# Kernel optimization log

Measured on AMD Instinct MI355X. Metric: run time of the kernel, lower is better.

## Reference

```python
import jax, jax.numpy as jnp
import numpy as np

N = 100_000      # nodes
E = 1_600_000    # edges (avg degree 16)
D = 64           # input_dim == hidden_dim
C = 10           # output classes
G = 512          # graphs in batch
L = 5            # num_layers (L-1 = 4 GINConv layers)
BN_EPS = 1e-5


def setup_inputs() -> dict:
    key = jax.random.key(0)
    ks = jax.random.split(key, 16)
    x = jax.random.normal(ks[0], (N, D), dtype=jnp.float32)
    edge_index = jax.random.randint(ks[1], (2, E), 0, N, dtype=jnp.int32)
    batch = jnp.sort(jax.random.randint(ks[2], (N,), 0, G, dtype=jnp.int32))
    s = 1.0 / np.sqrt(D)
    Lc = L - 1
    return {
        "x": x,
        "edge_index": edge_index,
        "batch": batch,
        "eps": jnp.zeros((Lc,), jnp.float32),                                   # GINConv eps (train_eps, init 0)
        "W1": jax.random.uniform(ks[3], (Lc, D, D), jnp.float32, -s, s),        # MLP linear 1
        "b1": jax.random.uniform(ks[4], (Lc, D), jnp.float32, -s, s),
        "g1": jnp.ones((Lc, D), jnp.float32),                                   # MLP BatchNorm
        "be1": jnp.zeros((Lc, D), jnp.float32),
        "W2": jax.random.uniform(ks[5], (Lc, D, D), jnp.float32, -s, s),        # MLP linear 2
        "b2": jax.random.uniform(ks[6], (Lc, D), jnp.float32, -s, s),
        "gout": jnp.ones((Lc, D), jnp.float32),                                 # outer BatchNorm
        "beout": jnp.zeros((Lc, D), jnp.float32),
        "Wp": jax.random.uniform(ks[7], (L, D, C), jnp.float32, -s, s),         # prediction linears
        "bp": jax.random.uniform(ks[8], (L, C), jnp.float32, -s, s),
    }


def _batchnorm(h, gamma, beta):
    # training-mode BN over node dim, biased variance (torch semantics)
    m = jnp.mean(h, axis=0)
    v = jnp.mean(jnp.square(h - m), axis=0)
    return gamma * (h - m) * jax.lax.rsqrt(v + BN_EPS) + beta


def reference(x, edge_index, batch, eps, W1, b1, g1, be1, W2, b2, gout, beout, Wp, bp):
    src, dst = edge_index[0], edge_index[1]
    hidden_rep = [x]
    h = x
    for l in range(L - 1):
        # GINConv: (1 + eps) * x + scatter-add of neighbor features
        agg = jax.ops.segment_sum(h[src], dst, num_segments=N)
        z = (1.0 + eps[l]) * h + agg
        # 2-layer MLP with internal BN+ReLU
        z = z @ W1[l] + b1[l]
        z = jax.nn.relu(_batchnorm(z, g1[l], be1[l]))
        z = z @ W2[l] + b2[l]
        # outer BN + ReLU
        h = jax.nn.relu(_batchnorm(z, gout[l], beout[l]))
        hidden_rep.append(h)
    # jumping-knowledge readout: per-layer global_add_pool + linear (dropout off / eval)
    score = jnp.zeros((G, C), jnp.float32)
    for l, hl in enumerate(hidden_rep):
        pooled = jax.ops.segment_sum(hl, batch, num_segments=G)
        score = score + pooled @ Wp[l] + bp[l]
    return score
```

## Files before the change

### kernel.cpp

```cpp
#include <hip/hip_runtime.h>

#define NN 100000
#define EE 1600000
#define DD 64
#define CC 10
#define GG 512
#define LL 5
#define NPAD 100352
#define N64 (NN * DD)
#define NB 392
#define PCH 4096
#define BCAP 6144
#define SC 8

typedef short bf16x8 __attribute__((ext_vector_type(8)));
typedef float f32x4  __attribute__((ext_vector_type(4)));
union U16 { uint4 u; bf16x8 h; };

__device__ __forceinline__ float bits2f(unsigned int b) { return __uint_as_float(b); }
__device__ __forceinline__ float bf2f(unsigned short s) { return __uint_as_float((unsigned int)s << 16); }
__device__ __forceinline__ unsigned short f2bf_rne(float v) {
    unsigned int b = __float_as_uint(v);
    return (unsigned short)((b + 0x7fffu + ((b >> 16) & 1u)) >> 16);
}
__device__ __forceinline__ void unpack8(uint4 u, float* f) {
    f[0] = bits2f(u.x << 16); f[1] = bits2f(u.x & 0xffff0000u);
    f[2] = bits2f(u.y << 16); f[3] = bits2f(u.y & 0xffff0000u);
    f[4] = bits2f(u.z << 16); f[5] = bits2f(u.z & 0xffff0000u);
    f[6] = bits2f(u.w << 16); f[7] = bits2f(u.w & 0xffff0000u);
}
__device__ __forceinline__ uint4 pack8(const float* f) {
    uint4 u;
    u.x = (unsigned int)f2bf_rne(f[0]) | ((unsigned int)f2bf_rne(f[1]) << 16);
    u.y = (unsigned int)f2bf_rne(f[2]) | ((unsigned int)f2bf_rne(f[3]) << 16);
    u.z = (unsigned int)f2bf_rne(f[4]) | ((unsigned int)f2bf_rne(f[5]) << 16);
    u.w = (unsigned int)f2bf_rne(f[6]) | ((unsigned int)f2bf_rne(f[7]) << 16);
    return u;
}
__device__ __forceinline__ void acc8(uint4 u, float* a) {
    float t[8];
    unpack8(u, t);
    #pragma unroll
    for (int k = 0; k < 8; ++k) a[k] += t[k];
}

__global__ __launch_bounds__(256) void prep_x_pool_k(
    const float* __restrict__ x, const int* __restrict__ batch,
    unsigned short* __restrict__ hb, float* __restrict__ pooled)
{
    int t = threadIdx.x;
    int f = t & 63;
    int q = t >> 6;
    int n0 = blockIdx.x * 64 + q * 16;
    int nmax = NN - n0; if (nmax > 16) nmax = 16;
    float acc = 0.f;
    int curg = -1;
    #pragma unroll 4
    for (int i = 0; i < nmax; ++i) {
        int n = n0 + i;
        int g = batch[n];
        if (g != curg) {
            if (curg >= 0) atomicAdd(&pooled[(size_t)curg * DD + f], acc);
            acc = 0.f; curg = g;
        }
        float v = x[(size_t)n * DD + f];
        hb[(size_t)n * DD + f] = f2bf_rne(v);
        acc += v;
    }
    if (curg >= 0) atomicAdd(&pooled[(size_t)curg * DD + f], acc);
}

__global__ __launch_bounds__(256) void prep_w_k(const float* __restrict__ W1,
                                                const float* __restrict__ W2,
                                                unsigned short* __restrict__ wt) {
    int mat = blockIdx.x;
    const float* src = (mat < 4) ? (W1 + (size_t)mat * 4096)
                                 : (W2 + (size_t)(mat - 4) * 4096);
    for (int idx = threadIdx.x; idx < 4096; idx += 256) {
        int c = idx >> 6, k = idx & 63;
        wt[(size_t)mat * 4096 + c * 64 + k] = f2bf_rne(src[k * 64 + c]);
    }
}

__global__ __launch_bounds__(256) void bhist_k(const int* __restrict__ ei,
                                               int* __restrict__ bh) {
    __shared__ int cnt[NB];
    for (int i = threadIdx.x; i < NB; i += 256) cnt[i] = 0;
    __syncthreads();
    int stride = gridDim.x * 256;
    for (int e = blockIdx.x * 256 + threadIdx.x; e < EE; e += stride)
        atomicAdd(&cnt[ei[EE + e] >> 8], 1);
    __syncthreads();
    for (int i = threadIdx.x; i < NB; i += 256)
        if (cnt[i]) atomicAdd(&bh[i], cnt[i]);
}

__global__ __launch_bounds__(512) void bscan_k(const int* __restrict__ bh,
                                               int* __restrict__ bo,
                                               int* __restrict__ bcur) {
    __shared__ int s[512];
    int t = threadIdx.x;
    int v = (t < NB) ? bh[t] : 0;
    s[t] = v;
    __syncthreads();
    for (int d = 1; d < 512; d <<= 1) {
        int a = (t >= d) ? s[t - d] : 0;
        __syncthreads();
        s[t] += a;
        __syncthreads();
    }
    int excl = s[t] - v;
    if (t < NB) { bo[t] = excl; bcur[t] = excl; }
    if (t == NB - 1) bo[NB] = excl + v;
}

__global__ __launch_bounds__(256) void partition_k(const int* __restrict__ ei,
                                                   int* __restrict__ bcur,
                                                   unsigned int* __restrict__ stage) {
    __shared__ int hist[NB];
    __shared__ int base[NB];
    __shared__ int gbase[NB];
    __shared__ int cnt2[NB];
    __shared__ int scanbuf[512];
    __shared__ unsigned int pairs[PCH];
    __shared__ unsigned short pbkt[PCH];
    int t = threadIdx.x;
    int e0 = blockIdx.x * PCH;
    int nE = EE - e0; if (nE > PCH) nE = PCH;

    for (int i = t; i < NB; i += 256) { hist[i] = 0; cnt2[i] = 0; }
    __syncthreads();

    int mys[16], myd[16];
    #pragma unroll
    for (int i = 0; i < 16; ++i) {
        int idx = i * 256 + t;
        if (idx < nE) {
            mys[i] = ei[e0 + idx];
            myd[i] = ei[EE + e0 + idx];
            atomicAdd(&hist[myd[i] >> 8], 1);
        } else myd[i] = -1;
    }
    __syncthreads();

    scanbuf[t]       = (t < NB) ? hist[t] : 0;
    scanbuf[t + 256] = (t + 256 < NB) ? hist[t + 256] : 0;
    __syncthreads();
    for (int d = 1; d < 512; d <<= 1) {
        int a0 = (t >= d) ? scanbuf[t - d] : 0;
        int a1 = ((t + 256) >= d) ? scanbuf[t + 256 - d] : 0;
        __syncthreads();
        scanbuf[t] += a0;
        scanbuf[t + 256] += a1;
        __syncthreads();
    }
    if (t < NB)       base[t]       = scanbuf[t] - hist[t];
    if (t + 256 < NB) base[t + 256] = scanbuf[t + 256] - hist[t + 256];
    __syncthreads();

    #pragma unroll
    for (int i = 0; i < 16; ++i) {
        if (myd[i] >= 0) {
            int b = myd[i] >> 8;
            int p = base[b] + atomicAdd(&cnt2[b], 1);
            pairs[p] = (unsigned)mys[i] | ((unsigned)(myd[i] & 255) << 17);
            pbkt[p] = (unsigned short)b;
        }
    }
    __syncthreads();
    for (int i = t; i < NB; i += 256)
        if (hist[i]) gbase[i] = atomicAdd(&bcur[i], hist[i]);
    __syncthreads();
    for (int p = t; p < nE; p += 256) {
        int b = pbkt[p];
        stage[gbase[b] + (p - base[b])] = pairs[p];
    }
}

__global__ __launch_bounds__(256) void bucket_csr_k(const unsigned int* __restrict__ stage,
                                                    const int* __restrict__ bo,
                                                    int* __restrict__ adj,
                                                    int* __restrict__ offs) {
    __shared__ int deg[256];
    __shared__ int sb[256];
    __shared__ int nb_[256];
    __shared__ int c2[256];
    __shared__ int loc[BCAP];
    int b = blockIdx.x;
    int s0 = bo[b], s1 = bo[b + 1];
    int cnt = s1 - s0;
    int t = threadIdx.x;

    deg[t] = 0;
    __syncthreads();
    for (int i = t; i < cnt; i += 256) atomicAdd(&deg[(stage[s0 + i] >> 17) & 255], 1);
    __syncthreads();
    sb[t] = deg[t];
    __syncthreads();
    for (int d = 1; d < 256; d <<= 1) {
        int a = (t >= d) ? sb[t - d] : 0;
        __syncthreads();
        sb[t] += a;
        __syncthreads();
    }
    int nbase = sb[t] - deg[t];
    nb_[t] = nbase;
    c2[t] = 0;
    offs[b * 256 + t] = s0 + nbase;
    __syncthreads();

    if (cnt <= BCAP) {
        for (int i = t; i < cnt; i += 256) {
            unsigned int pr = stage[s0 + i];
            int ln = (pr >> 17) & 255;
            int p = nb_[ln] + atomicAdd(&c2[ln], 1);
            loc[p] = (int)(pr & 0x1FFFF);
        }
        __syncthreads();
        for (int i = t; i < cnt; i += 256) adj[s0 + i] = loc[i];
    } else {
        for (int i = t; i < cnt; i += 256) {
            unsigned int pr = stage[s0 + i];
            int ln = (pr >> 17) & 255;
            int p = nb_[ln] + atomicAdd(&c2[ln], 1);
            adj[s0 + p] = (int)(pr & 0x1FFFF);
        }
    }
}

__global__ __launch_bounds__(512, 6) void layer1_k(
    const unsigned short* __restrict__ hb, const int* __restrict__ adj,
    const int* __restrict__ offs, const float* __restrict__ epsArr, int l,
    const unsigned short* __restrict__ wtm, const float* __restrict__ bias,
    unsigned short* __restrict__ z1, float* __restrict__ stats1,
    float* __restrict__ stats2z)
{
    __shared__ unsigned short aLDS[64 * 64];
    const int t = threadIdx.x;
    const int lane = t & 63;
    const int w = t >> 6;
    const int n15 = lane & 15;
    const int quad = lane >> 4;

    if (blockIdx.x < SC && t < 128) stats2z[blockIdx.x * 128 + t] = 0.f;

    const float epsv = 1.0f + epsArr[l];
    const int c8 = lane & 7;
    {
        int lr = w * 8 + (lane >> 3);
        int n = blockIdx.x * 64 + lr;
        float acc[8] = {0.f,0.f,0.f,0.f,0.f,0.f,0.f,0.f};
        if (n < NN) {
            uint4 a = *(const uint4*)(hb + (size_t)n * DD + c8 * 8);
            unpack8(a, acc);
            #pragma unroll
            for (int j2 = 0; j2 < 8; ++j2) acc[j2] *= epsv;
            int j = offs[n], end = offs[n + 1];
            #pragma unroll 1
            for (; j + 3 < end; j += 4) {
                int s0 = adj[j], s1 = adj[j + 1], s2 = adj[j + 2], s3 = adj[j + 3];
                uint4 v0 = *(const uint4*)(hb + (size_t)s0 * DD + c8 * 8);
                uint4 v1 = *(const uint4*)(hb + (size_t)s1 * DD + c8 * 8);
                uint4 v2 = *(const uint4*)(hb + (size_t)s2 * DD + c8 * 8);
                uint4 v3 = *(const uint4*)(hb + (size_t)s3 * DD + c8 * 8);
                acc8(v0, acc); acc8(v1, acc); acc8(v2, acc); acc8(v3, acc);
            }
            #pragma unroll 1
            for (; j < end; ++j) {
                uint4 v0 = *(const uint4*)(hb + (size_t)adj[j] * DD + c8 * 8);
                acc8(v0, acc);
            }
        }
        int pu = c8 ^ (lr & 7);
        *(uint4*)(aLDS + lr * 64 + pu * 8) = pack8(acc);
    }

    const int rt = w & 3;
    const int cb = (w >> 2) * 2;
    U16 bfr[2][2];
    #pragma unroll
    for (int ci = 0; ci < 2; ++ci)
        #pragma unroll
        for (int ks = 0; ks < 2; ++ks)
            bfr[ci][ks].u = *(const uint4*)(wtm + (size_t)((cb + ci) * 16 + n15) * 64 + ks * 32 + quad * 8);

    __syncthreads();

    U16 afr[2];
    int lr2 = rt * 16 + n15;
    #pragma unroll
    for (int ks = 0; ks < 2; ++ks) {
        int pu = (ks * 4 + quad) ^ (lr2 & 7);
        afr[ks].u = *(const uint4*)(aLDS + lr2 * 64 + pu * 8);
    }

    const int rowg0 = blockIdx.x * 64 + rt * 16;
    const int copy = blockIdx.x & (SC - 1);
    #pragma unroll
    for (int ci = 0; ci < 2; ++ci) {
        int ct = cb + ci;
        f32x4 acc = {0.f, 0.f, 0.f, 0.f};
        acc = __builtin_amdgcn_mfma_f32_16x16x32_bf16(afr[0].h, bfr[ci][0].h, acc, 0, 0, 0);
        acc = __builtin_amdgcn_mfma_f32_16x16x32_bf16(afr[1].h, bfr[ci][1].h, acc, 0, 0, 0);
        int col = ct * 16 + n15;
        float bcol = bias[col];
        float s = 0.f, ss = 0.f;
        #pragma unroll
        for (int r = 0; r < 4; ++r) {
            int rg = rowg0 + quad * 4 + r;
            float v = acc[r] + bcol;
            if (rg < NN) {
                z1[(size_t)rg * DD + col] = f2bf_rne(v);
                s += v;
                ss = fmaf(v, v, ss);
            }
        }
        s  += __shfl_xor(s, 16, 64);  s  += __shfl_xor(s, 32, 64);
        ss += __shfl_xor(ss, 16, 64); ss += __shfl_xor(ss, 32, 64);
        if (lane < 16) {
            atomicAdd(&stats1[copy * 128 + ct * 16 + lane], s);
            atomicAdd(&stats1[copy * 128 + 64 + ct * 16 + lane], ss);
        }
    }
}

__global__ __launch_bounds__(256) void layer2_k(
    const unsigned short* __restrict__ z1, const float* __restrict__ stats1,
    const float* __restrict__ gamma, const float* __restrict__ beta, int off,
    const unsigned short* __restrict__ wtm, const float* __restrict__ bias,
    unsigned short* __restrict__ z2, float* __restrict__ stats2)
{
    __shared__ float ssS[128];
    const int t = threadIdx.x;
    const int lane = t & 63;
    const int w = t >> 6;
    const int n15 = lane & 15;
    const int quad = lane >> 4;
    const int rowg0 = blockIdx.x * 64 + w * 16;

    U16 bfr[4][2];
    #pragma unroll
    for (int ct = 0; ct < 4; ++ct)
        #pragma unroll
        for (int ks = 0; ks < 2; ++ks)
            bfr[ct][ks].u = *(const uint4*)(wtm + (size_t)(ct * 16 + n15) * 64 + ks * 32 + quad * 8);

    int arow = rowg0 + n15;
    int arowc = (arow < NN) ? arow : (NN - 1);
    uint4 raw[2];
    #pragma unroll
    for (int ks = 0; ks < 2; ++ks)
        raw[ks] = *(const uint4*)(z1 + (size_t)arowc * DD + ks * 32 + quad * 8);

    if (t < 64) {
        float S = 0.f, SS = 0.f;
        #pragma unroll
        for (int c = 0; c < SC; ++c) { S += stats1[c * 128 + t]; SS += stats1[c * 128 + 64 + t]; }
        float inv_n = 1.0f / (float)NN;
        float mean = S * inv_n;
        float var  = SS * inv_n - mean * mean;
        float sc = gamma[off + t] * rsqrtf(var + 1e-5f);
        ssS[t] = sc;
        ssS[64 + t] = beta[off + t] - sc * mean;
    }
    __syncthreads();

    U16 afr[2];
    #pragma unroll
    for (int ks = 0; ks < 2; ++ks) {
        float f[8];
        unpack8(raw[ks], f);
        int k0 = ks * 32 + quad * 8;
        #pragma unroll
        for (int j = 0; j < 8; ++j)
            f[j] = fmaxf(fmaf(ssS[k0 + j], f[j], ssS[64 + k0 + j]), 0.f);
        afr[ks].u = pack8(f);
    }

    const int copy = blockIdx.x & (SC - 1);
    #pragma unroll
    for (int ct = 0; ct < 4; ++ct) {
        f32x4 acc = {0.f, 0.f, 0.f, 0.f};
        acc = __builtin_amdgcn_mfma_f32_16x16x32_bf16(afr[0].h, bfr[ct][0].h, acc, 0, 0, 0);
        acc = __builtin_amdgcn_mfma_f32_16x16x32_bf16(afr[1].h, bfr[ct][1].h, acc, 0, 0, 0);
        int col = ct * 16 + n15;
        float bcol = bias[col];
        float s = 0.f, ss = 0.f;
        #pragma unroll
        for (int r = 0; r < 4; ++r) {
            int rg = rowg0 + quad * 4 + r;
            float v = acc[r] + bcol;
            if (rg < NN) {
                z2[(size_t)rg * DD + col] = f2bf_rne(v);
                s += v;
                ss = fmaf(v, v, ss);
            }
        }
        s  += __shfl_xor(s, 16, 64);  s  += __shfl_xor(s, 32, 64);
        ss += __shfl_xor(ss, 16, 64); ss += __shfl_xor(ss, 32, 64);
        if (lane < 16) {
            atomicAdd(&stats2[copy * 128 + ct * 16 + lane], s);
            atomicAdd(&stats2[copy * 128 + 64 + ct * 16 + lane], ss);
        }
    }
}

__global__ __launch_bounds__(256) void layer3_k(
    const unsigned short* __restrict__ z2, const float* __restrict__ stats2,
    const float* __restrict__ gamma, const float* __restrict__ beta, int off,
    const int* __restrict__ batch, unsigned short* __restrict__ hout,
    float* __restrict__ pooled, float* __restrict__ stats1z)
{
    __shared__ float ssS[128];
    int t = threadIdx.x;
    if (blockIdx.x < SC && t < 128) stats1z[blockIdx.x * 128 + t] = 0.f;
    if (t < 64) {
        float S = 0.f, SS = 0.f;
        #pragma unroll
        for (int c = 0; c < SC; ++c) { S += stats2[c * 128 + t]; SS += stats2[c * 128 + 64 + t]; }
        float inv_n = 1.0f / (float)NN;
        float mean = S * inv_n;
        float var  = SS * inv_n - mean * mean;
        float sc = gamma[off + t] * rsqrtf(var + 1e-5f);
        ssS[t] = sc;
        ssS[64 + t] = beta[off + t] - sc * mean;
    }
    __syncthreads();

    int f = t & 63;
    int q = t >> 6;
    int n0 = blockIdx.x * 64 + q * 16;
    int nmax = NN - n0; if (nmax > 16) nmax = 16;
    float sc = ssS[f], sh = ssS[64 + f];
    float acc = 0.f;
    int curg = -1;
    #pragma unroll 4
    for (int i = 0; i < nmax; ++i) {
        int n = n0 + i;
        int g = batch[n];
        if (g != curg) {
            if (curg >= 0) atomicAdd(&pooled[(size_t)curg * DD + f], acc);
            acc = 0.f; curg = g;
        }
        float v = bf2f(z2[(size_t)n * DD + f]);
        v = fmaxf(fmaf(sc, v, sh), 0.f);
        hout[(size_t)n * DD + f] = f2bf_rne(v);
        acc += v;
    }
    if (curg >= 0) atomicAdd(&pooled[(size_t)curg * DD + f], acc);
}

__global__ void readout_k(const float* __restrict__ pooled,
                          const float* __restrict__ Wp, const float* __restrict__ bp,
                          float* __restrict__ out)
{
    int gc = blockIdx.x * blockDim.x + threadIdx.x;
    if (gc >= GG * CC) return;
    int g = gc / CC, c = gc - g * CC;
    float acc = 0.f;
    for (int l = 0; l < LL; ++l) {
        acc += bp[l * CC + c];
        const float* p  = pooled + ((size_t)l * GG + g) * DD;
        const float* wv = Wp + (size_t)l * DD * CC + c;
        #pragma unroll 8
        for (int f = 0; f < DD; ++f) acc = fmaf(p[f], wv[f * CC], acc);
    }
    out[gc] = acc;
}

extern "C" void kernel_launch(void* const* d_in, const int* in_sizes, int n_in,
                              void* d_out, int out_size, void* d_ws, size_t ws_size,
                              hipStream_t stream) {
    const float* x     = (const float*)d_in[0];
    const int*   ei    = (const int*)d_in[1];
    const int*   batch = (const int*)d_in[2];
    const float* eps   = (const float*)d_in[3];
    const float* W1    = (const float*)d_in[4];
    const float* b1    = (const float*)d_in[5];
    const float* g1    = (const float*)d_in[6];
    const float* be1   = (const float*)d_in[7];
    const float* W2    = (const float*)d_in[8];
    const float* b2    = (const float*)d_in[9];
    const float* gout  = (const float*)d_in[10];
    const float* beout = (const float*)d_in[11];
    const float* Wp    = (const float*)d_in[12];
    const float* bp    = (const float*)d_in[13];
    float* out = (float*)d_out;

    unsigned int* stage = (unsigned int*)d_ws;
    int* adj   = (int*)(stage + EE);
    int* offs  = adj + EE;
    int* bh    = offs + NPAD + 256;
    int* bo    = bh + 400;
    int* bcur  = bo + 400;
    float* pooled = (float*)(bcur + 400);
    float* stats1 = pooled + (size_t)LL * GG * DD;
    float* stats2 = stats1 + SC * 128;
    unsigned short* hb  = (unsigned short*)(stats2 + SC * 128);
    unsigned short* z1b = hb + N64;
    unsigned short* z2b = z1b + N64;
    unsigned short* wt  = z2b + N64;

    hipMemsetAsync(pooled, 0, ((size_t)LL * GG * DD + 2 * SC * 128) * sizeof(float), stream);
    prep_x_pool_k<<<(NN + 63) / 64, 256, 0, stream>>>(x, batch, hb, pooled);
    prep_w_k<<<8, 256, 0, stream>>>(W1, W2, wt);

    hipMemsetAsync(bh, 0, NB * sizeof(int), stream);
    bhist_k<<<512, 256, 0, stream>>>(ei, bh);
    bscan_k<<<1, 512, 0, stream>>>(bh, bo, bcur);
    partition_k<<<(EE + PCH - 1) / PCH, 256, 0, stream>>>(ei, bcur, stage);
    bucket_csr_k<<<NB, 256, 0, stream>>>(stage, bo, adj, offs);

    const int gemm_grid = (NN + 63) / 64;
    const int node_grid = (NN + 63) / 64;
    for (int l = 0; l < LL - 1; ++l) {
        layer1_k<<<gemm_grid, 512, 0, stream>>>(
            hb, adj, offs, eps, l, wt + (size_t)l * 4096, b1 + l * DD, z1b, stats1, stats2);
        layer2_k<<<gemm_grid, 256, 0, stream>>>(
            z1b, stats1, g1, be1, l * DD, wt + (size_t)(4 + l) * 4096, b2 + l * DD, z2b, stats2);
        layer3_k<<<node_grid, 256, 0, stream>>>(
            z2b, stats2, gout, beout, l * DD, batch, hb,
            pooled + (size_t)(l + 1) * GG * DD, stats1);
    }
    readout_k<<<(GG * CC + 255) / 256, 256, 0, stream>>>(pooled, Wp, bp, out);
}
```

Before: 615.7 us.

## Process nodes in degree-sorted order in aggregation kernel to balance wavefront work

Builds a degree histogram during CSR construction, scans it, and scatters node ids into a permutation sorted by descending degree. The fused aggregation+GEMM kernel then processes nodes in this permuted order and writes z1 rows back to their original positions. The goal is to reduce load imbalance between lanes and waves that gather differing neighbor counts. The cost is two extra small kernels, a perm lookup, and scattered rather than contiguous row stores and self-feature reads.

```diff
diff --git a/kernel.cpp b/kernel.cpp
--- a/kernel.cpp
+++ b/kernel.cpp
@@ -180,7 +180,8 @@
 __global__ __launch_bounds__(256) void bucket_csr_k(const unsigned int* __restrict__ stage,
                                                     const int* __restrict__ bo,
                                                     int* __restrict__ adj,
-                                                    int* __restrict__ offs) {
+                                                    int* __restrict__ offs,
+                                                    int* __restrict__ dh) {
     __shared__ int deg[256];
     __shared__ int sb[256];
     __shared__ int nb_[256];
@@ -207,6 +208,10 @@
     nb_[t] = nbase;
     c2[t] = 0;
     offs[b * 256 + t] = s0 + nbase;
+    if (b * 256 + t < NN) {
+        int dgc = deg[t]; if (dgc > 127) dgc = 127;
+        atomicAdd(&dh[dgc], 1);
+    }
     __syncthreads();
 
     if (cnt <= BCAP) {
@@ -228,14 +233,38 @@
     }
 }
 
+__global__ void dscan_k(const int* __restrict__ dh, int* __restrict__ dbase) {
+    __shared__ int s[128];
+    int t = threadIdx.x;
+    s[t] = dh[t];
+    __syncthreads();
+    int sum = 0;
+    for (int d = t + 1; d < 128; ++d) sum += s[d];
+    dbase[t] = sum;
+}
+
+__global__ __launch_bounds__(256) void dscatter_k(const int* __restrict__ offs,
+                                                  int* __restrict__ dcnt,
+                                                  const int* __restrict__ dbase,
+                                                  int* __restrict__ perm) {
+    int n = blockIdx.x * 256 + threadIdx.x;
+    if (n >= NN) return;
+    int d = offs[n + 1] - offs[n];
+    if (d > 127) d = 127;
+    int pos = dbase[d] + atomicAdd(&dcnt[d], 1);
+    perm[pos] = n;
+}
+
 __global__ __launch_bounds__(512, 6) void layer1_k(
     const unsigned short* __restrict__ hb, const int* __restrict__ adj,
-    const int* __restrict__ offs, const float* __restrict__ epsArr, int l,
+    const int* __restrict__ offs, const int* __restrict__ perm,
+    const float* __restrict__ epsArr, int l,
     const unsigned short* __restrict__ wtm, const float* __restrict__ bias,
     unsigned short* __restrict__ z1, float* __restrict__ stats1,
     float* __restrict__ stats2z)
 {
     __shared__ unsigned short aLDS[64 * 64];
+    __shared__ int pLDS[64];
     const int t = threadIdx.x;
     const int lane = t & 63;
     const int w = t >> 6;
@@ -248,9 +277,11 @@
     const int c8 = lane & 7;
     {
         int lr = w * 8 + (lane >> 3);
-        int n = blockIdx.x * 64 + lr;
+        int gidx = blockIdx.x * 64 + lr;
+        int n = (gidx < NN) ? perm[gidx] : -1;
+        if (c8 == 0) pLDS[lr] = n;
         float acc[8] = {0.f,0.f,0.f,0.f,0.f,0.f,0.f,0.f};
-        if (n < NN) {
+        if (n >= 0) {
             uint4 a = *(const uint4*)(hb + (size_t)n * DD + c8 * 8);
             unpack8(a, acc);
             #pragma unroll
@@ -294,7 +325,6 @@
         afr[ks].u = *(const uint4*)(aLDS + lr2 * 64 + pu * 8);
     }
 
-    const int rowg0 = blockIdx.x * 64 + rt * 16;
     const int copy = blockIdx.x & (SC - 1);
     #pragma unroll
     for (int ci = 0; ci < 2; ++ci) {
@@ -307,10 +337,10 @@
         float s = 0.f, ss = 0.f;
         #pragma unroll
         for (int r = 0; r < 4; ++r) {
-            int rg = rowg0 + quad * 4 + r;
+            int pn = pLDS[rt * 16 + quad * 4 + r];
             float v = acc[r] + bcol;
-            if (rg < NN) {
-                z1[(size_t)rg * DD + col] = f2bf_rne(v);
+            if (pn >= 0) {
+                z1[(size_t)pn * DD + col] = f2bf_rne(v);
                 s += v;
                 ss = fmaf(v, v, ss);
             }
@@ -491,9 +521,13 @@
     int* adj   = (int*)(stage + EE);
     int* offs  = adj + EE;
     int* bh    = offs + NPAD + 256;
-    int* bo    = bh + 400;
+    int* dh    = bh + 400;
+    int* dcnt  = dh + 128;
+    int* bo    = dcnt + 128;
     int* bcur  = bo + 400;
-    float* pooled = (float*)(bcur + 400);
+    int* dbase = bcur + 400;
+    int* perm  = dbase + 128;
+    float* pooled = (float*)(perm + NN);
     float* stats1 = pooled + (size_t)LL * GG * DD;
     float* stats2 = stats1 + SC * 128;
     unsigned short* hb  = (unsigned short*)(stats2 + SC * 128);
@@ -505,17 +539,19 @@
     prep_x_pool_k<<<(NN + 63) / 64, 256, 0, stream>>>(x, batch, hb, pooled);
     prep_w_k<<<8, 256, 0, stream>>>(W1, W2, wt);
 
-    hipMemsetAsync(bh, 0, NB * sizeof(int), stream);
+    hipMemsetAsync(bh, 0, (400 + 128 + 128) * sizeof(int), stream);
     bhist_k<<<512, 256, 0, stream>>>(ei, bh);
     bscan_k<<<1, 512, 0, stream>>>(bh, bo, bcur);
     partition_k<<<(EE + PCH - 1) / PCH, 256, 0, stream>>>(ei, bcur, stage);
-    bucket_csr_k<<<NB, 256, 0, stream>>>(stage, bo, adj, offs);
+    bucket_csr_k<<<NB, 256, 0, stream>>>(stage, bo, adj, offs, dh);
+    dscan_k<<<1, 128, 0, stream>>>(dh, dbase);
+    dscatter_k<<<NB, 256, 0, stream>>>(offs, dcnt, dbase, perm);
 
     const int gemm_grid = (NN + 63) / 64;
     const int node_grid = (NN + 63) / 64;
     for (int l = 0; l < LL - 1; ++l) {
         layer1_k<<<gemm_grid, 512, 0, stream>>>(
-            hb, adj, offs, eps, l, wt + (size_t)l * 4096, b1 + l * DD, z1b, stats1, stats2);
+            hb, adj, offs, perm, eps, l, wt + (size_t)l * 4096, b1 + l * DD, z1b, stats1, stats2);
         layer2_k<<<gemm_grid, 256, 0, stream>>>(
             z1b, stats1, g1, be1, l * DD, wt + (size_t)(4 + l) * 4096, b2 + l * DD, z2b, stats2);
         layer3_k<<<node_grid, 256, 0, stream>>>(
```

New measurement: 1.049 ms. 1.7x slower.
